# Optimization experiments

Measured on AMD Instinct MI355X. Metric: run time of the kernel, lower is better.

## Reference

```python
import jax, jax.numpy as jnp
import numpy as np

EPS = 1e-5

def bn(x, g, b, m, v):
    # inference-mode BatchNorm2d over channel dim
    return (x - m[None, :, None, None]) * jax.lax.rsqrt(v[None, :, None, None] + EPS) * g[None, :, None, None] + b[None, :, None, None]

def conv1x1(x, W, b=None):
    y = jnp.einsum('oc,bchw->bohw', W, x)
    return y + b[None, :, None, None] if b is not None else y

def forward(x, W3, b3, g1, b1, m1, v1, Wa, ba, g2, b2, m2, v2, Wq, bq, Wk, bk, Wv, bv, gam, Wg, bg, g3, b3n, m3, v3, Wf, bf, g4, b4, m4, v4, Wr, rs):
    B, C, H, Wd = x.shape
    N = H * Wd
    # conv branch: 3x3 conv + BN + ReLU
    y3 = jax.lax.conv_general_dilated(x, W3, (1, 1), ((1, 1), (1, 1)), dimension_numbers=('NCHW', 'OIHW', 'NCHW'))
    local = jax.nn.relu(bn(y3 + b3[None, :, None, None], g1, b1, m1, v1))
    # attn branch: 1x1 conv + BN + ReLU, then full-resolution attention
    a = jax.nn.relu(bn(conv1x1(x, Wa, ba), g2, b2, m2, v2))
    q = conv1x1(a, Wq, bq).reshape(B, -1, N)   # [B, C/8, N]
    k = conv1x1(a, Wk, bk).reshape(B, -1, N)   # [B, C/8, N]
    v = conv1x1(a, Wv, bv).reshape(B, -1, N)   # [B, C, N]
    att = jax.nn.softmax(jnp.einsum('bcn,bcm->bnm', q, k), axis=-1)  # [B, N, N], unscaled as in source
    o = jnp.einsum('bcm,bnm->bcn', v, att).reshape(a.shape)
    attn_feat = gam * o + a
    # gated fusion
    combined = jnp.concatenate([local, attn_feat], axis=1)
    gate = jax.nn.sigmoid(bn(conv1x1(combined, Wg, bg), g3, b3n, m3, v3))
    fused = gate * local + (1.0 - gate) * attn_feat
    out = jax.nn.relu(bn(conv1x1(jnp.concatenate([fused, combined], axis=1), Wf, bf), g4, b4, m4, v4))
    res = conv1x1(x, Wr)  # residual 1x1 conv, no bias (in != out channels)
    return out + rs * res

def setup_inputs() -> dict:
    B, Ci, Co, H, W_ = 4, 64, 128, 64, 64
    Cq = Co // 8
    ks = jax.random.split(jax.random.key(0), 24)
    def rn(i, s, sc=0.05):
        return jax.random.normal(ks[i], s, jnp.float32) * sc
    def var(i, c):
        return jax.random.uniform(ks[i], (c,), jnp.float32, 0.5, 1.5)
    ones = lambda c: jnp.ones((c,), jnp.float32)
    zeros = lambda c: jnp.zeros((c,), jnp.float32)
    return {
        'x': rn(0, (B, Ci, H, W_), 1.0),
        'W3': rn(1, (Co, Ci, 3, 3)), 'b3': rn(2, (Co,)),
        'g1': ones(Co), 'b1': zeros(Co), 'm1': rn(3, (Co,), 0.1), 'v1': var(4, Co),
        'Wa': rn(5, (Co, Ci)), 'ba': rn(6, (Co,)),
        'g2': ones(Co), 'b2': zeros(Co), 'm2': rn(7, (Co,), 0.1), 'v2': var(8, Co),
        'Wq': rn(9, (Cq, Co)), 'bq': rn(10, (Cq,)),
        'Wk': rn(11, (Cq, Co)), 'bk': rn(12, (Cq,)),
        'Wv': rn(13, (Co, Co)), 'bv': rn(14, (Co,)),
        'gam': jnp.array(0.5, jnp.float32),
        'Wg': rn(15, (Co, 2 * Co)), 'bg': rn(16, (Co,)),
        'g3': ones(Co), 'b3n': zeros(Co), 'm3': rn(17, (Co,), 0.1), 'v3': var(18, Co),
        'Wf': rn(19, (Co, 3 * Co)), 'bf': rn(20, (Co,)),
        'g4': ones(Co), 'b4': zeros(Co), 'm4': rn(21, (Co,), 0.1), 'v4': var(22, Co),
        'Wr': rn(23, (Co, Ci)),
        'rs': jnp.array(0.1, jnp.float32),
    }

def reference(x, W3, b3, g1, b1, m1, v1, Wa, ba, g2, b2, m2, v2, Wq, bq, Wk, bk, Wv, bv, gam, Wg, bg, g3, b3n, m3, v3, Wf, bf, g4, b4, m4, v4, Wr, rs):
    return forward(x, W3, b3, g1, b1, m1, v1, Wa, ba, g2, b2, m2, v2, Wq, bq, Wk, bk, Wv, bv, gam, Wg, bg, g3, b3n, m3, v3, Wf, bf, g4, b4, m4, v4, Wr, rs)
```

## Files before the change

### kernel.cpp

```cpp
#include <hip/hip_runtime.h>
#include <hip/hip_bf16.h>

#define CI_ 64
#define CO_ 128
#define NPIX 4096
#define CQ_ 16
#define EPS_ 1e-5f

typedef __attribute__((ext_vector_type(8))) __bf16 bf16x8;
typedef __attribute__((ext_vector_type(4))) __bf16 bf16x4;
typedef __attribute__((ext_vector_type(4))) float f32x4;

__global__ __launch_bounds__(256) void z_prepx(
    const float* __restrict__ x, __bf16* __restrict__ xT)
{
    __shared__ float tl[64][65];
    int b = blockIdx.x >> 6;
    int n0 = (blockIdx.x & 63) * 64;
    int tid = threadIdx.x;
    int nn = tid & 63, c4 = tid >> 6;
#pragma unroll
    for (int p = 0; p < 16; ++p) {
        int ci = p * 4 + c4;
        tl[ci][nn] = x[((size_t)b * CI_ + ci) * NPIX + n0 + nn];
    }
    __syncthreads();
#pragma unroll
    for (int p = 0; p < 2; ++p) {
        int idx = p * 256 + tid;
        int n = idx >> 3, cig = idx & 7;
        bf16x8 vv;
#pragma unroll
        for (int j = 0; j < 8; ++j) vv[j] = (__bf16)tl[cig * 8 + j][n];
        ((bf16x8*)xT)[((size_t)b * NPIX + n0 + n) * 8 + cig] = vv;
    }
}

__global__ __launch_bounds__(256) void z_prepw(
    const float* __restrict__ W3, __bf16* __restrict__ Wt2)
{
    int o = blockIdx.x * 256 + threadIdx.x;
    int co = o / 576;
    int r = o - co * 576;
    int tap = r >> 6;
    int ci = r & 63;
    Wt2[o] = (__bf16)W3[((size_t)co * CI_ + ci) * 9 + tap];
}

__global__ __launch_bounds__(256) void z_prepfw2(
    const float* __restrict__ Wg, const float* __restrict__ Wf, const float* __restrict__ Wr,
    const float* __restrict__ Wa, const float* __restrict__ Wq, const float* __restrict__ Wk,
    const float* __restrict__ Wv, __bf16* __restrict__ Wb)
{
    int i = blockIdx.x * 256 + threadIdx.x;
    if (i >= 118784) return;
    float val;
    if (i < 32768) val = Wg[i];
    else if (i < 81920) val = Wf[i - 32768];
    else if (i < 90112) val = Wr[i - 81920];
    else if (i < 98304) val = Wa[i - 90112];
    else if (i < 100352) val = Wq[i - 98304];
    else if (i < 102400) val = Wk[i - 100352];
    else val = Wv[i - 102400];
    Wb[i] = (__bf16)val;
}

__global__ __launch_bounds__(256) void z_mega(
    const __bf16* __restrict__ xT, const __bf16* __restrict__ Wb,
    const float* __restrict__ ba, const float* __restrict__ g2, const float* __restrict__ b2,
    const float* __restrict__ m2, const float* __restrict__ v2,
    const float* __restrict__ bq, const float* __restrict__ bk, const float* __restrict__ bv,
    float* __restrict__ a, float* __restrict__ q, __bf16* __restrict__ kT, __bf16* __restrict__ V2)
{
    __shared__ __align__(16) __bf16 an[16 * 128];
    int tid = threadIdx.x;
    int b = blockIdx.x >> 8;
    int n0 = (blockIdx.x & 255) * 16;
    int l = tid & 63, w = tid >> 6;
    int lm = l & 15, g = l >> 4;

    const __bf16* Wa2 = Wb + 90112;
    const __bf16* Wq2 = Wb + 98304;
    const __bf16* Wk2 = Wb + 100352;
    const __bf16* Wv2 = Wb + 102400;

    bf16x8 bx[2];
#pragma unroll
    for (int kc = 0; kc < 2; ++kc)
        bx[kc] = ((const bf16x8*)xT)[((size_t)b * NPIX + n0 + lm) * 8 + (kc * 4 + g)];
    f32x4 pa[2];
#pragma unroll
    for (int ct = 0; ct < 2; ++ct) {
#pragma unroll
        for (int r = 0; r < 4; ++r) pa[ct][r] = ba[w * 32 + ct * 16 + g * 4 + r];
#pragma unroll
        for (int kc = 0; kc < 2; ++kc) {
            bf16x8 afr = *(const bf16x8*)&Wa2[(size_t)(w * 32 + ct * 16 + lm) * 64 + kc * 32 + g * 8];
            pa[ct] = __builtin_amdgcn_mfma_f32_16x16x32_bf16(afr, bx[kc], pa[ct], 0, 0, 0);
        }
    }
#pragma unroll
    for (int ct = 0; ct < 2; ++ct) {
        bf16x4 pk;
#pragma unroll
        for (int r = 0; r < 4; ++r) {
            int co = w * 32 + ct * 16 + g * 4 + r;
            float sc = rsqrtf(v2[co] + EPS_) * g2[co];
            float sh = b2[co] - m2[co] * sc;
            float y = fmaxf(pa[ct][r] * sc + sh, 0.f);
            a[((size_t)b * CO_ + co) * NPIX + n0 + lm] = y;
            pk[r] = (__bf16)y;
        }
        int co8 = w * 4 + ct * 2 + (g >> 1);
        int ch = co8 ^ (lm & 7);
        *(bf16x4*)&an[lm * 128 + ch * 8 + (g & 1) * 4] = pk;
    }
    __syncthreads();

    bf16x8 bn[4];
#pragma unroll
    for (int kc = 0; kc < 4; ++kc) {
        int ch = (kc * 4 + g) ^ (lm & 7);
        bn[kc] = *(const bf16x8*)&an[lm * 128 + ch * 8];
    }
    f32x4 pv[2];
#pragma unroll
    for (int ct = 0; ct < 2; ++ct) {
#pragma unroll
        for (int r = 0; r < 4; ++r) pv[ct][r] = bv[w * 32 + ct * 16 + g * 4 + r];
#pragma unroll
        for (int kc = 0; kc < 4; ++kc) {
            bf16x8 afr = *(const bf16x8*)&Wv2[(size_t)(w * 32 + ct * 16 + lm) * 128 + kc * 32 + g * 8];
            pv[ct] = __builtin_amdgcn_mfma_f32_16x16x32_bf16(afr, bn[kc], pv[ct], 0, 0, 0);
        }
    }
    int n = n0 + lm;
#pragma unroll
    for (int ct = 0; ct < 2; ++ct)
#pragma unroll
        for (int r = 0; r < 4; ++r) {
            int c = w * 32 + ct * 16 + g * 4 + r;
            V2[(size_t)b * 524288 + (size_t)(n >> 3) * 1024 + c * 8 + (n & 7)] = (__bf16)pv[ct][r];
        }
    if (w == 0) {
        f32x4 pq;
#pragma unroll
        for (int r = 0; r < 4; ++r) pq[r] = bq[g * 4 + r];
#pragma unroll
        for (int kc = 0; kc < 4; ++kc) {
            bf16x8 afr = *(const bf16x8*)&Wq2[(size_t)lm * 128 + kc * 32 + g * 8];
            pq = __builtin_amdgcn_mfma_f32_16x16x32_bf16(afr, bn[kc], pq, 0, 0, 0);
        }
#pragma unroll
        for (int r = 0; r < 4; ++r)
            q[((size_t)b * CQ_ + g * 4 + r) * NPIX + n] = pq[r];
    } else if (w == 1) {
        f32x4 pk2;
#pragma unroll
        for (int r = 0; r < 4; ++r) pk2[r] = bk[g * 4 + r];
#pragma unroll
        for (int kc = 0; kc < 4; ++kc) {
            bf16x8 afr = *(const bf16x8*)&Wk2[(size_t)lm * 128 + kc * 32 + g * 8];
            pk2 = __builtin_amdgcn_mfma_f32_16x16x32_bf16(afr, bn[kc], pk2, 0, 0, 0);
        }
        bf16x4 kk;
#pragma unroll
        for (int r = 0; r < 4; ++r) kk[r] = (__bf16)pk2[r];
        *(bf16x4*)&kT[((size_t)b * NPIX + n) * CQ_ + g * 4] = kk;
    }
}

__global__ __launch_bounds__(256) void z_conv3m(
    const __bf16* __restrict__ xT, const __bf16* __restrict__ Wt2,
    const float* __restrict__ b3, const float* __restrict__ g,
    const float* __restrict__ bb, const float* __restrict__ m,
    const float* __restrict__ v, float* __restrict__ local)
{
    __shared__ __align__(16) __bf16 xt[3 * 66 * 64];
    __shared__ __align__(16) __bf16 wt[32 * 576];
    __shared__ float scs[32], shs[32];

    int blk = blockIdx.x;
    int b = blk >> 8;
    int h = (blk >> 2) & 63;
    int cg = blk & 3;
    int co0 = cg * 32;
    int tid = threadIdx.x;
    int l = tid & 63;
    int nt = tid >> 6;
    int lm = l & 15, lh = l >> 4;

    if (tid < 32) {
        int co = co0 + tid;
        float scv = rsqrtf(v[co] + EPS_) * g[co];
        scs[tid] = scv;
        shs[tid] = (b3[co] - m[co]) * scv + bb[co];
    }

    const bf16x8* xs = (const bf16x8*)xT + (size_t)b * (NPIX * 8);
    for (int i = tid; i < 1584; i += 256) {
        int r = i / 528;
        int rem = i - r * 528;
        int c = rem >> 3;
        int cig = rem & 7;
        int hh = h + r - 1;
        int gc = c - 1;
        bf16x8 val;
#pragma unroll
        for (int j = 0; j < 8; ++j) val[j] = (__bf16)0.f;
        if ((unsigned)hh < 64u && (unsigned)gc < 64u)
            val = xs[(hh * 64 + gc) * 8 + cig];
        *(bf16x8*)&xt[(r * 66 + c) * 64 + ((cig ^ (c & 7)) * 8)] = val;
    }
    const bf16x8* wsrc = (const bf16x8*)Wt2 + (size_t)co0 * 72;
    for (int i = tid; i < 2304; i += 256) {
        int co = i / 72;
        int kc = i - co * 72;
        *(bf16x8*)&wt[co * 576 + ((kc ^ (co & 7)) * 8)] = wsrc[i];
    }
    __syncthreads();

    f32x4 acc0 = {0.f, 0.f, 0.f, 0.f};
    f32x4 acc1 = {0.f, 0.f, 0.f, 0.f};
#pragma unroll
    for (int tap = 0; tap < 9; ++tap) {
        int dh = tap / 3, dw = tap % 3;
#pragma unroll
        for (int ks = 0; ks < 2; ++ks) {
            int cig = ks * 4 + lh;
            int col = nt * 16 + lm + dw;
            bf16x8 bfr = *(const bf16x8*)&xt[(dh * 66 + col) * 64 + ((cig ^ (col & 7)) * 8)];
            int kcg = tap * 8 + cig;
            bf16x8 a0 = *(const bf16x8*)&wt[lm * 576 + ((kcg ^ (lm & 7)) * 8)];
            bf16x8 a1 = *(const bf16x8*)&wt[(16 + lm) * 576 + ((kcg ^ (lm & 7)) * 8)];
            acc0 = __builtin_amdgcn_mfma_f32_16x16x32_bf16(a0, bfr, acc0, 0, 0, 0);
            acc1 = __builtin_amdgcn_mfma_f32_16x16x32_bf16(a1, bfr, acc1, 0, 0, 0);
        }
    }

    size_t obase = (size_t)b * CO_ * NPIX + h * 64 + nt * 16 + lm;
#pragma unroll
    for (int r = 0; r < 4; ++r) {
        int cl0 = lh * 4 + r;
        float y0 = fmaxf(acc0[r] * scs[cl0] + shs[cl0], 0.f);
        local[obase + (size_t)(co0 + cl0) * NPIX] = y0;
        int cl1 = 16 + cl0;
        float y1 = fmaxf(acc1[r] * scs[cl1] + shs[cl1], 0.f);
        local[obase + (size_t)(co0 + cl1) * NPIX] = y1;
    }
}

__global__ __launch_bounds__(256) void z_attn4(
    const float* __restrict__ q, const __bf16* __restrict__ kT, const __bf16* __restrict__ V2,
    const float* __restrict__ a, const float* __restrict__ gamp, float* __restrict__ attn)
{
    __shared__ __align__(16) unsigned char smem[8704];
    __shared__ float wmax[4][16], wsum[4][16], fs[16];
    __bf16* p_lds = (__bf16*)smem;
    float* o_lds = (float*)smem;

    int tid = threadIdx.x;
    int b = blockIdx.x >> 8;
    int q0 = (blockIdx.x & 255) * 16;
    int l = tid & 63;
    int w = tid >> 6;
    int lm = l & 15;
    int g = l >> 4;

    bf16x8 qfrag;
#pragma unroll
    for (int j = 0; j < 8; ++j) qfrag[j] = (__bf16)0.f;
    if (g < 2) {
#pragma unroll
        for (int j = 0; j < 8; ++j)
            qfrag[j] = (__bf16)q[((size_t)b * CQ_ + g * 8 + j) * NPIX + q0 + lm];
    }

    float m_run = -1e30f, l_run = 0.f;
    f32x4 acc0 = {0.f, 0.f, 0.f, 0.f};
    f32x4 acc1 = {0.f, 0.f, 0.f, 0.f};
    int c0 = w * 32 + lm;
    int c1 = c0 + 16;
    const bf16x8* vbase = (const bf16x8*)V2 + (size_t)b * 65536;
    const __bf16* ktb = kT + (size_t)b * NPIX * CQ_;

    for (int t = 0; t < 16; ++t) {
        int m0 = t * 256;
        f32x4 sfr[4];
#pragma unroll
        for (int ms = 0; ms < 4; ++ms) {
            bf16x8 kf;
#pragma unroll
            for (int j = 0; j < 8; ++j) kf[j] = (__bf16)0.f;
            if (g < 2)
                kf = *(const bf16x8*)&ktb[(size_t)(m0 + w * 64 + ms * 16 + lm) * CQ_ + g * 8];
            f32x4 zz = {0.f, 0.f, 0.f, 0.f};
            sfr[ms] = __builtin_amdgcn_mfma_f32_16x16x32_bf16(kf, qfrag, zz, 0, 0, 0);
        }
        float pmax = -1e30f;
#pragma unroll
        for (int ms = 0; ms < 4; ++ms)
#pragma unroll
            for (int r = 0; r < 4; ++r) pmax = fmaxf(pmax, sfr[ms][r]);
        pmax = fmaxf(pmax, __shfl_xor(pmax, 16));
        pmax = fmaxf(pmax, __shfl_xor(pmax, 32));
        if (g == 0) wmax[w][lm] = pmax;
        __syncthreads();
        float tmax = fmaxf(fmaxf(wmax[0][lm], wmax[1][lm]), fmaxf(wmax[2][lm], wmax[3][lm]));
        float nm = fmaxf(m_run, tmax);
        float f = __expf(m_run - nm);
        m_run = nm;
        if (w == 0 && g == 0) fs[lm] = f;
        float psum = 0.f;
#pragma unroll
        for (int ms = 0; ms < 4; ++ms) {
            float p0 = __expf(sfr[ms][0] - nm);
            float p1 = __expf(sfr[ms][1] - nm);
            float p2 = __expf(sfr[ms][2] - nm);
            float p3 = __expf(sfr[ms][3] - nm);
            psum += (p0 + p1) + (p2 + p3);
            bf16x4 pk;
            pk[0] = (__bf16)p0; pk[1] = (__bf16)p1; pk[2] = (__bf16)p2; pk[3] = (__bf16)p3;
            *(bf16x4*)&p_lds[lm * 264 + w * 64 + ms * 16 + g * 4] = pk;
        }
        psum += __shfl_xor(psum, 16);
        psum += __shfl_xor(psum, 32);
        if (g == 0) wsum[w][lm] = psum;
        __syncthreads();
        float tsum = (wsum[0][lm] + wsum[1][lm]) + (wsum[2][lm] + wsum[3][lm]);
        l_run = l_run * f + tsum;
        float f0 = fs[g * 4 + 0], f1 = fs[g * 4 + 1], f2 = fs[g * 4 + 2], f3 = fs[g * 4 + 3];
        acc0[0] *= f0; acc0[1] *= f1; acc0[2] *= f2; acc0[3] *= f3;
        acc1[0] *= f0; acc1[1] *= f1; acc1[2] *= f2; acc1[3] *= f3;
#pragma unroll
        for (int ks = 0; ks < 8; ++ks) {
            bf16x8 afrag = *(const bf16x8*)&p_lds[lm * 264 + ks * 32 + g * 8];
            int msv = (m0 >> 3) + ks * 4 + g;
            bf16x8 bf0 = vbase[msv * 128 + c0];
            bf16x8 bf1 = vbase[msv * 128 + c1];
            acc0 = __builtin_amdgcn_mfma_f32_16x16x32_bf16(afrag, bf0, acc0, 0, 0, 0);
            acc1 = __builtin_amdgcn_mfma_f32_16x16x32_bf16(afrag, bf1, acc1, 0, 0, 0);
        }
        __syncthreads();
    }

#pragma unroll
    for (int r = 0; r < 4; ++r) {
        int qrow = g * 4 + r;
        o_lds[c0 * 17 + qrow] = acc0[r];
        o_lds[c1 * 17 + qrow] = acc1[r];
    }
    __syncthreads();
    float gam = gamp[0];
    int qi = tid & 15;
    float inv = 1.f / l_run;
#pragma unroll
    for (int j = 0; j < 8; ++j) {
        int cc = (tid >> 4) + 16 * j;
        size_t idx = ((size_t)b * CO_ + cc) * NPIX + q0 + qi;
        attn[idx] = gam * (o_lds[cc * 17 + qi] * inv) + a[idx];
    }
}

__global__ __launch_bounds__(256) void z_fuseout2(
    const float* __restrict__ local, const float* __restrict__ attn, const float* __restrict__ x,
    const __bf16* __restrict__ Wb,
    const float* __restrict__ bg, const float* __restrict__ g3, const float* __restrict__ b3n,
    const float* __restrict__ m3, const float* __restrict__ v3,
    const float* __restrict__ bfb, const float* __restrict__ g4, const float* __restrict__ b4,
    const float* __restrict__ m4, const float* __restrict__ v4,
    const float* __restrict__ rsp, float* __restrict__ out)
{
    __shared__ __align__(16) unsigned char smem[32768 + 4096];
    __bf16* sb2 = (__bf16*)smem;
    __bf16* sxT = (__bf16*)(smem + 28672);

    int tid = threadIdx.x;
    int b = blockIdx.x >> 7;
    int n0 = (blockIdx.x & 127) * 32;

#pragma unroll
    for (int p = 0; p < 4; ++p) {
        int idx = p * 256 + tid;
        int c = idx >> 3, j = idx & 7;
        float lv[4], av[4];
        *(float4*)lv = *(const float4*)(local + ((size_t)b * CO_ + c) * NPIX + n0 + j * 4);
        *(float4*)av = *(const float4*)(attn + ((size_t)b * CO_ + c) * NPIX + n0 + j * 4);
#pragma unroll
        for (int e = 0; e < 4; ++e) {
            int n = j * 4 + e;
            int k1 = 128 + c, k2 = 256 + c;
            sb2[n * 448 + (((k1 >> 3) ^ (n & 7)) << 3) + (k1 & 7)] = (__bf16)lv[e];
            sb2[n * 448 + (((k2 >> 3) ^ (n & 7)) << 3) + (k2 & 7)] = (__bf16)av[e];
        }
    }
#pragma unroll
    for (int p = 0; p < 2; ++p) {
        int idx = p * 256 + tid;
        int c = idx >> 3, j = idx & 7;
        float xv[4];
        *(float4*)xv = *(const float4*)(x + ((size_t)b * CI_ + c) * NPIX + n0 + j * 4);
#pragma unroll
        for (int e = 0; e < 4; ++e) {
            int n = j * 4 + e;
            sxT[n * 64 + (((c >> 3) ^ (n & 7)) << 3) + (c & 7)] = (__bf16)xv[e];
        }
    }
    __syncthreads();

    int l = tid & 63, w = tid >> 6;
    int lm = l & 15, g = l >> 4;
    int co0 = w * 32;
    int t7 = lm & 7;

    f32x4 p1[2][2];
#pragma unroll
    for (int cs = 0; cs < 2; ++cs) {
        float bv = bg[co0 + cs * 16 + lm];
#pragma unroll
        for (int ns = 0; ns < 2; ++ns) {
            p1[ns][cs][0] = bv; p1[ns][cs][1] = bv; p1[ns][cs][2] = bv; p1[ns][cs][3] = bv;
        }
    }
    const __bf16* Wg2 = Wb;
#pragma unroll
    for (int kc = 0; kc < 8; ++kc) {
        int ch = (16 + kc * 4 + g) ^ t7;
        bf16x8 a0 = *(const bf16x8*)&sb2[lm * 448 + ch * 8];
        bf16x8 a1 = *(const bf16x8*)&sb2[(16 + lm) * 448 + ch * 8];
        bf16x8 b0 = *(const bf16x8*)&Wg2[(size_t)(co0 + lm) * 256 + kc * 32 + g * 8];
        bf16x8 b1 = *(const bf16x8*)&Wg2[(size_t)(co0 + 16 + lm) * 256 + kc * 32 + g * 8];
        p1[0][0] = __builtin_amdgcn_mfma_f32_16x16x32_bf16(a0, b0, p1[0][0], 0, 0, 0);
        p1[0][1] = __builtin_amdgcn_mfma_f32_16x16x32_bf16(a0, b1, p1[0][1], 0, 0, 0);
        p1[1][0] = __builtin_amdgcn_mfma_f32_16x16x32_bf16(a1, b0, p1[1][0], 0, 0, 0);
        p1[1][1] = __builtin_amdgcn_mfma_f32_16x16x32_bf16(a1, b1, p1[1][1], 0, 0, 0);
    }
#pragma unroll
    for (int cs = 0; cs < 2; ++cs) {
        int co = co0 + cs * 16 + lm;
        float sc3 = rsqrtf(v3[co] + EPS_) * g3[co];
        float sh3 = b3n[co] - m3[co] * sc3;
        int kl = 128 + co, ka = 256 + co;
#pragma unroll
        for (int ns = 0; ns < 2; ++ns)
#pragma unroll
            for (int r = 0; r < 4; ++r) {
                int n = ns * 16 + g * 4 + r;
                float z = p1[ns][cs][r] * sc3 + sh3;
                float gate = 1.f / (1.f + __expf(-z));
                float lv = (float)sb2[n * 448 + (((kl >> 3) ^ (n & 7)) << 3) + (kl & 7)];
                float av = (float)sb2[n * 448 + (((ka >> 3) ^ (n & 7)) << 3) + (ka & 7)];
                float fu = gate * lv + (1.f - gate) * av;
                sb2[n * 448 + (((co >> 3) ^ (n & 7)) << 3) + (co & 7)] = (__bf16)fu;
            }
    }
    __syncthreads();

    f32x4 p2[2][2], pr[2][2];
#pragma unroll
    for (int cs = 0; cs < 2; ++cs) {
        float bv = bfb[co0 + cs * 16 + lm];
#pragma unroll
        for (int ns = 0; ns < 2; ++ns) {
            p2[ns][cs][0] = bv; p2[ns][cs][1] = bv; p2[ns][cs][2] = bv; p2[ns][cs][3] = bv;
            pr[ns][cs] = (f32x4){0.f, 0.f, 0.f, 0.f};
        }
    }
    const __bf16* Wf2 = Wb + 32768;
    const __bf16* Wr2 = Wb + 81920;
#pragma unroll
    for (int kc = 0; kc < 12; ++kc) {
        int ch = (kc * 4 + g) ^ t7;
        bf16x8 a0 = *(const bf16x8*)&sb2[lm * 448 + ch * 8];
        bf16x8 a1 = *(const bf16x8*)&sb2[(16 + lm) * 448 + ch * 8];
        bf16x8 b0 = *(const bf16x8*)&Wf2[(size_t)(co0 + lm) * 384 + kc * 32 + g * 8];
        bf16x8 b1 = *(const bf16x8*)&Wf2[(size_t)(co0 + 16 + lm) * 384 + kc * 32 + g * 8];
        p2[0][0] = __builtin_amdgcn_mfma_f32_16x16x32_bf16(a0, b0, p2[0][0], 0, 0, 0);
        p2[0][1] = __builtin_amdgcn_mfma_f32_16x16x32_bf16(a0, b1, p2[0][1], 0, 0, 0);
        p2[1][0] = __builtin_amdgcn_mfma_f32_16x16x32_bf16(a1, b0, p2[1][0], 0, 0, 0);
        p2[1][1] = __builtin_amdgcn_mfma_f32_16x16x32_bf16(a1, b1, p2[1][1], 0, 0, 0);
    }
#pragma unroll
    for (int kc = 0; kc < 2; ++kc) {
        int ch = (kc * 4 + g) ^ t7;
        bf16x8 a0 = *(const bf16x8*)&sxT[lm * 64 + ch * 8];
        bf16x8 a1 = *(const bf16x8*)&sxT[(16 + lm) * 64 + ch * 8];
        bf16x8 b0 = *(const bf16x8*)&Wr2[(size_t)(co0 + lm) * 64 + kc * 32 + g * 8];
        bf16x8 b1 = *(const bf16x8*)&Wr2[(size_t)(co0 + 16 + lm) * 64 + kc * 32 + g * 8];
        pr[0][0] = __builtin_amdgcn_mfma_f32_16x16x32_bf16(a0, b0, pr[0][0], 0, 0, 0);
        pr[0][1] = __builtin_amdgcn_mfma_f32_16x16x32_bf16(a0, b1, pr[0][1], 0, 0, 0);
        pr[1][0] = __builtin_amdgcn_mfma_f32_16x16x32_bf16(a1, b0, pr[1][0], 0, 0, 0);
        pr[1][1] = __builtin_amdgcn_mfma_f32_16x16x32_bf16(a1, b1, pr[1][1], 0, 0, 0);
    }
    __syncthreads();

    float* o_lds = (float*)smem;
    float rsv = rsp[0];
#pragma unroll
    for (int cs = 0; cs < 2; ++cs) {
        int co = co0 + cs * 16 + lm;
        float sc4 = rsqrtf(v4[co] + EPS_) * g4[co];
        float sh4 = b4[co] - m4[co] * sc4;
#pragma unroll
        for (int ns = 0; ns < 2; ++ns)
#pragma unroll
            for (int r = 0; r < 4; ++r) {
                int n = ns * 16 + g * 4 + r;
                float o = fmaxf(p2[ns][cs][r] * sc4 + sh4, 0.f) + rsv * pr[ns][cs][r];
                o_lds[co * 36 + n] = o;
            }
    }
    __syncthreads();
    {
        int c = tid >> 1, h = tid & 1;
#pragma unroll
        for (int j2 = 0; j2 < 4; ++j2) {
            float4 vv = *(float4*)&o_lds[c * 36 + h * 16 + j2 * 4];
            *(float4*)(out + ((size_t)b * CO_ + c) * NPIX + n0 + h * 16 + j2 * 4) = vv;
        }
    }
}

extern "C" void kernel_launch(void* const* d_in, const int* in_sizes, int n_in,
                              void* d_out, int out_size, void* d_ws, size_t ws_size,
                              hipStream_t stream) {
    const float* x   = (const float*)d_in[0];
    const float* W3  = (const float*)d_in[1];
    const float* b3  = (const float*)d_in[2];
    const float* g1  = (const float*)d_in[3];
    const float* b1  = (const float*)d_in[4];
    const float* m1  = (const float*)d_in[5];
    const float* v1  = (const float*)d_in[6];
    const float* Wa  = (const float*)d_in[7];
    const float* ba  = (const float*)d_in[8];
    const float* g2  = (const float*)d_in[9];
    const float* b2  = (const float*)d_in[10];
    const float* m2  = (const float*)d_in[11];
    const float* v2  = (const float*)d_in[12];
    const float* Wq  = (const float*)d_in[13];
    const float* bq  = (const float*)d_in[14];
    const float* Wk  = (const float*)d_in[15];
    const float* bk  = (const float*)d_in[16];
    const float* Wv  = (const float*)d_in[17];
    const float* bv  = (const float*)d_in[18];
    const float* gam = (const float*)d_in[19];
    const float* Wg  = (const float*)d_in[20];
    const float* bg  = (const float*)d_in[21];
    const float* g3  = (const float*)d_in[22];
    const float* b3n = (const float*)d_in[23];
    const float* m3  = (const float*)d_in[24];
    const float* v3  = (const float*)d_in[25];
    const float* Wf  = (const float*)d_in[26];
    const float* bfb = (const float*)d_in[27];
    const float* g4  = (const float*)d_in[28];
    const float* b4  = (const float*)d_in[29];
    const float* m4  = (const float*)d_in[30];
    const float* v4  = (const float*)d_in[31];
    const float* Wr  = (const float*)d_in[32];
    const float* rs  = (const float*)d_in[33];

    float* ws    = (float*)d_ws;
    float* a_    = ws;
    float* local = ws + 2097152;
    float* attn  = ws + 4194304;
    __bf16* V2   = (__bf16*)(ws + 6291456);
    float* q     = ws + 7340032;
    __bf16* kT   = (__bf16*)(ws + 7602176);
    __bf16* xT   = (__bf16*)(ws + 7864320);
    __bf16* Wt2  = (__bf16*)(ws + 8388608);
    __bf16* Wb   = (__bf16*)(ws + 8450048);

    float* out = (float*)d_out;

    z_prepx<<<256, 256, 0, stream>>>(x, xT);
    z_prepw<<<288, 256, 0, stream>>>(W3, Wt2);
    z_prepfw2<<<464, 256, 0, stream>>>(Wg, Wf, Wr, Wa, Wq, Wk, Wv, Wb);
    z_mega<<<1024, 256, 0, stream>>>(xT, Wb, ba, g2, b2, m2, v2, bq, bk, bv, a_, q, kT, V2);
    z_attn4<<<1024, 256, 0, stream>>>(q, kT, V2, a_, gam, attn);
    z_conv3m<<<1024, 256, 0, stream>>>(xT, Wt2, b3, g1, b1, m1, v1, local);
    z_fuseout2<<<512, 256, 0, stream>>>(local, attn, x, Wb, bg, g3, b3n, m3, v3,
                                        bfb, g4, b4, m4, v4, rs, out);
}
```

Baseline: 117.7 us.

## Split attention over key dimension into two halves with combine kernel

```diff
diff --git a/kernel.cpp b/kernel.cpp
--- a/kernel.cpp
+++ b/kernel.cpp
@@ -250,9 +250,9 @@
     }
 }
 
-__global__ __launch_bounds__(256) void z_attn4(
+__global__ __launch_bounds__(256) void z_attn4s(
     const float* __restrict__ q, const __bf16* __restrict__ kT, const __bf16* __restrict__ V2,
-    const float* __restrict__ a, const float* __restrict__ gamp, float* __restrict__ attn)
+    __bf16* __restrict__ o_part, float2* __restrict__ ml)
 {
     __shared__ __align__(16) unsigned char smem[8704];
     __shared__ float wmax[4][16], wsum[4][16], fs[16];
@@ -260,7 +260,8 @@
     float* o_lds = (float*)smem;
 
     int tid = threadIdx.x;
-    int b = blockIdx.x >> 8;
+    int b = blockIdx.x >> 9;
+    int half = (blockIdx.x >> 8) & 1;
     int q0 = (blockIdx.x & 255) * 16;
     int l = tid & 63;
     int w = tid >> 6;
@@ -284,8 +285,8 @@
     const bf16x8* vbase = (const bf16x8*)V2 + (size_t)b * 65536;
     const __bf16* ktb = kT + (size_t)b * NPIX * CQ_;
 
-    for (int t = 0; t < 16; ++t) {
-        int m0 = t * 256;
+    for (int t = 0; t < 8; ++t) {
+        int m0 = half * 2048 + t * 256;
         f32x4 sfr[4];
 #pragma unroll
         for (int ms = 0; ms < 4; ++ms) {
@@ -350,16 +351,44 @@
         o_lds[c0 * 17 + qrow] = acc0[r];
         o_lds[c1 * 17 + qrow] = acc1[r];
     }
-    __syncthreads();
-    float gam = gamp[0];
+    if (w == 0 && g == 0)
+        ml[(size_t)(half * 4 + b) * NPIX + q0 + lm] = make_float2(m_run, l_run);
+    __syncthreads();
     int qi = tid & 15;
     float inv = 1.f / l_run;
 #pragma unroll
     for (int j = 0; j < 8; ++j) {
         int cc = (tid >> 4) + 16 * j;
-        size_t idx = ((size_t)b * CO_ + cc) * NPIX + q0 + qi;
-        attn[idx] = gam * (o_lds[cc * 17 + qi] * inv) + a[idx];
-    }
+        size_t idx = ((size_t)(half * 4 + b) * CO_ + cc) * NPIX + q0 + qi;
+        o_part[idx] = (__bf16)(o_lds[cc * 17 + qi] * inv);
+    }
+}
+
+__global__ __launch_bounds__(256) void z_acomb(
+    const __bf16* __restrict__ o_part, const float2* __restrict__ ml,
+    const float* __restrict__ a, const float* __restrict__ gamp, float* __restrict__ attn)
+{
+    int i = blockIdx.x * 256 + threadIdx.x;
+    int n4 = (i & 1023) * 4;
+    int co = (i >> 10) & (CO_ - 1);
+    int b = i >> 17;
+    float gam = gamp[0];
+    bf16x4 o1 = *(const bf16x4*)&o_part[((size_t)b * CO_ + co) * NPIX + n4];
+    bf16x4 o2 = *(const bf16x4*)&o_part[((size_t)(4 + b) * CO_ + co) * NPIX + n4];
+    float4 av = *(const float4*)(a + ((size_t)b * CO_ + co) * NPIX + n4);
+    float r[4], ai[4] = {av.x, av.y, av.z, av.w};
+#pragma unroll
+    for (int e = 0; e < 4; ++e) {
+        float2 m1 = ml[(size_t)b * NPIX + n4 + e];
+        float2 m2 = ml[(size_t)(4 + b) * NPIX + n4 + e];
+        float mm = fmaxf(m1.x, m2.x);
+        float w1 = m1.y * __expf(m1.x - mm);
+        float w2 = m2.y * __expf(m2.x - mm);
+        float o = ((float)o1[e] * w1 + (float)o2[e] * w2) / (w1 + w2);
+        r[e] = gam * o + ai[e];
+    }
+    float4 rv = {r[0], r[1], r[2], r[3]};
+    *(float4*)(attn + ((size_t)b * CO_ + co) * NPIX + n4) = rv;
 }
 
 __global__ __launch_bounds__(256) void z_fuseout2(
@@ -569,6 +598,8 @@
     __bf16* xT   = (__bf16*)(ws + 7864320);
     __bf16* Wt2  = (__bf16*)(ws + 8388608);
     __bf16* Wb   = (__bf16*)(ws + 8450048);
+    __bf16* o_part = (__bf16*)(ws + 8509440);
+    float2* ml   = (float2*)(ws + 10606592);
 
     float* out = (float*)d_out;
 
@@ -576,7 +607,8 @@
     z_prepw<<<288, 256, 0, stream>>>(W3, Wt2);
     z_prepfw2<<<464, 256, 0, stream>>>(Wg, Wf, Wr, Wa, Wq, Wk, Wv, Wb);
     z_mega<<<1024, 256, 0, stream>>>(xT, Wb, ba, g2, b2, m2, v2, bq, bk, bv, a_, q, kT, V2);
-    z_attn4<<<1024, 256, 0, stream>>>(q, kT, V2, a_, gam, attn);
+    z_attn4s<<<2048, 256, 0, stream>>>(q, kT, V2, o_part, ml);
+    z_acomb<<<2048, 256, 0, stream>>>(o_part, ml, a_, gam, attn);
     z_conv3m<<<1024, 256, 0, stream>>>(xT, Wt2, b3, g1, b1, m1, v1, local);
     z_fuseout2<<<512, 256, 0, stream>>>(local, attn, x, Wb, bg, g3, b3n, m3, v3,
                                         bfb, g4, b4, m4, v4, rs, out);
```

Measured after the change: 122.5 us. +4.1%, slower.
